# Optimization experiments

Hardware: AMD Instinct MI355X
Metric: run time of the kernel (lower is better)

The kernel has to match this reference:

```python
import jax, jax.numpy as jnp
import numpy as np

B, D, N = 8192, 1024, 4096     # batch, input_dim, num_outputs
SEG, W_SEG = 256, 16           # 256 uniform segments of width 16 (SEG*W_SEG == N)
TAU = 0.2                      # gumbel-softmax temperature


def setup_inputs() -> dict:
    key = jax.random.key(0)
    k1, k2, k3, k4 = jax.random.split(key, 4)
    bound = 1.0 / np.sqrt(D)   # init_bounded from the original module
    x = jax.random.normal(k1, (B, D), jnp.float32)
    W = jax.random.uniform(k2, (D, N), jnp.float32, -bound, bound)
    b = jax.random.uniform(k3, (N,), jnp.float32, -bound, bound)
    # Standard Gumbel(0,1) noise, precomputed for determinism: g = -log(-log(U))
    u = jax.random.uniform(k4, (B, N), jnp.float32, 1e-10, 1.0)
    gumbel = -jnp.log(-jnp.log(u))
    # segment flags: 0 -> tanh, nonzero -> gumbel-softmax (alternating)
    flags = (jnp.arange(SEG) % 2).astype(jnp.int32)
    return {"x": x, "W": W, "b": b, "gumbel": gumbel, "flags": flags}


def reference(x, W, b, gumbel, flags):
    # Dense layer
    outputs = x @ W + b                        # [B, N]
    # Segments are uniform-width, so the per-segment slice loop collapses to a reshape.
    y = outputs.reshape(B, SEG, W_SEG)         # [B, SEG, W_SEG]
    g = gumbel.reshape(B, SEG, W_SEG)
    # gumbel-softmax over each segment (hard=False path of the original)
    soft = jax.nn.softmax((y + g) / TAU, axis=-1)
    # per-segment dispatch: flag==0 -> tanh, else gumbel-softmax
    data_t = jnp.where(flags[None, :, None] == 0, jnp.tanh(y), soft)
    return outputs, data_t.reshape(B, N)
```

## Files before the change

kernel.cpp:

```cpp
#include <hip/hip_runtime.h>
#include <hip/hip_bf16.h>

#define B_DIM 8192
#define D_DIM 1024
#define N_DIM 4096
#define TAU_INV 5.0f

typedef __bf16 bf16x8 __attribute__((ext_vector_type(8)));
typedef __bf16 bf16x4 __attribute__((ext_vector_type(4)));
typedef float  f32x4  __attribute__((ext_vector_type(4)));

__device__ __forceinline__ void gld_lds16(const void* g, void* l) {
  __builtin_amdgcn_global_load_lds((const __attribute__((address_space(1))) void*)g,
                                   (__attribute__((address_space(3))) void*)l,
                                   16, 0, 0);
}
__device__ __forceinline__ float fast_rcp(float x) {
  return __builtin_amdgcn_rcpf(x);
}
#define MFMA(a, b, c) __builtin_amdgcn_mfma_f32_16x16x32_bf16((a), (b), (c), 0, 0, 0)

__global__ void prep_w(const float* __restrict__ W, __bf16* __restrict__ wht) {
  __shared__ float tile[32][33];
  const int tn = blockIdx.x & 127;
  const int tk = blockIdx.x >> 7;
  const int tx = threadIdx.x & 31;
  const int ty = threadIdx.x >> 5;
#pragma unroll
  for (int r = 0; r < 4; ++r) {
    const int k = tk * 32 + ty + r * 8;
    tile[ty + r * 8][tx] = W[(size_t)k * N_DIM + tn * 32 + tx];
  }
  __syncthreads();
#pragma unroll
  for (int r = 0; r < 4; ++r) {
    const int nn = tn * 32 + ty + r * 8;
    const int kk = tk * 32 + tx;
    wht[(size_t)nn * D_DIM + kk] = (__bf16)tile[tx][ty + r * 8];
  }
}

#define BM 128
#define BN 256
#define BK 32
#define THREADS 512

__global__ __launch_bounds__(THREADS, 4) void gemm_fused(
    const float* __restrict__ x,
    const __bf16* __restrict__ wht,
    const float* __restrict__ bias, const float* __restrict__ gumbel,
    const int* __restrict__ flags, float* __restrict__ out) {
  __shared__ __align__(16) __bf16 As[2][BM * BK];
  __shared__ __align__(16) __bf16 Bs[2][BN * BK];
  float* Ebuf = reinterpret_cast<float*>(&Bs[0][0]);

  const int tid  = threadIdx.x;
  const int lane = tid & 63;
  const int wave = tid >> 6;
  const int wr   = wave >> 2;
  const int wc   = wave & 3;
  const int fr   = lane & 15;
  const int q4   = lane >> 4;
  const int prot8 = ((q4 + ((fr >> 1) & 3)) & 3) * 8;

  const int bx  = blockIdx.x;
  const int xcd = bx & 7;
  const int ii  = bx >> 3;
  const int tn  = ii >> 3;
  const int tm  = xcd * 8 + (ii & 7);
  const int row0 = tm * BM;
  const int col0 = tn * BN;

  const int r0 = tid >> 2;
  const int l8 = (((tid & 3) - ((tid >> 3) & 3)) & 3) * 8;

  const float*  Axf = x   + (size_t)row0 * D_DIM;
  const __bf16* Bsc = wht + (size_t)col0 * D_DIM;

  f32x4 a0_, a1_;

#define ALOAD(t_)                                                            \
  do {                                                                       \
    const size_t o_ = (size_t)r0 * D_DIM + (t_) * 32 + l8;                   \
    a0_ = *reinterpret_cast<const f32x4*>(Axf + o_);                         \
    a1_ = *reinterpret_cast<const f32x4*>(Axf + o_ + 4);                     \
  } while (0)

#define CVTW(b)                                                              \
  do {                                                                       \
    bf16x8 h_;                                                               \
    h_[0] = (__bf16)a0_[0]; h_[1] = (__bf16)a0_[1];                          \
    h_[2] = (__bf16)a0_[2]; h_[3] = (__bf16)a0_[3];                          \
    h_[4] = (__bf16)a1_[0]; h_[5] = (__bf16)a1_[1];                          \
    h_[6] = (__bf16)a1_[2]; h_[7] = (__bf16)a1_[3];                          \
    *reinterpret_cast<bf16x8*>(&As[b][tid * 8]) = h_;                        \
  } while (0)

#define BGLD(b, t_)                                                          \
  do {                                                                       \
    const int ko_ = (t_) * 32;                                               \
    gld_lds16(Bsc + (size_t)r0 * D_DIM + ko_ + l8, &Bs[b][tid * 8]);         \
    gld_lds16(Bsc + (size_t)(128 + r0) * D_DIM + ko_ + l8,                   \
              &Bs[b][(512 + tid) * 8]);                                      \
  } while (0)

#define COMPUTE(b)                                                           \
  {                                                                          \
    bf16x8 bfr_[4];                                                          \
    _Pragma("unroll")                                                        \
    for (int n = 0; n < 4; ++n)                                              \
      bfr_[n] = *reinterpret_cast<const bf16x8*>(                            \
          &Bs[b][(wc * 64 + n * 16 + fr) * BK + prot8]);                     \
    __builtin_amdgcn_s_setprio(1);                                           \
    _Pragma("unroll")                                                        \
    for (int m = 0; m < 4; ++m) {                                            \
      const bf16x8 av_ = *reinterpret_cast<const bf16x8*>(                   \
          &As[b][(wr * 64 + m * 16 + fr) * BK + prot8]);                     \
      _Pragma("unroll")                                                      \
      for (int n = 0; n < 4; ++n)                                            \
        acc[m][n] = MFMA(bfr_[n], av_, acc[m][n]);                           \
    }                                                                        \
    __builtin_amdgcn_s_setprio(0);                                           \
  }

  f32x4 acc[4][4];
#pragma unroll
  for (int m = 0; m < 4; ++m)
#pragma unroll
    for (int n = 0; n < 4; ++n) acc[m][n] = (f32x4){0.f, 0.f, 0.f, 0.f};

  ALOAD(0);
  BGLD(0, 0);
  CVTW(0);
  __syncthreads();

#pragma unroll 1
  for (int it = 0; it < 15; ++it) {
    ALOAD(2 * it + 1); BGLD(1, 2 * it + 1);
    COMPUTE(0)
    CVTW(1);
    __syncthreads();
    ALOAD(2 * it + 2); BGLD(0, 2 * it + 2);
    COMPUTE(1)
    CVTW(0);
    __syncthreads();
  }
  ALOAD(31); BGLD(1, 31);
  COMPUTE(0)
  CVTW(1);
  __syncthreads();
  COMPUTE(1)

  float* out0 = out;
  float* out1 = out + (size_t)B_DIM * N_DIM;

  const int tcol = tid & 63;
  const int gcol = col0 + tcol * 4;
  const float4 bias4 = *reinterpret_cast<const float4*>(bias + gcol);
  const int flag = flags[(col0 >> 4) + (tcol >> 2)];

#pragma unroll
  for (int ck = 0; ck < 4; ++ck) {
    __syncthreads();
    if (wr == (ck >> 1)) {
#pragma unroll
      for (int mi = 0; mi < 2; ++mi) {
        const int lrow = mi * 16 + fr;
        const int m = (ck & 1) * 2 + mi;
#pragma unroll
        for (int n = 0; n < 4; ++n) {
          const int s = (wc * 16 + n * 4 + q4) ^ (lrow & 7);
          *reinterpret_cast<f32x4*>(&Ebuf[lrow * 256 + s * 4]) = acc[m][n];
        }
      }
    }
    __syncthreads();
#pragma unroll
    for (int rr = 0; rr < 4; ++rr) {
      const int lrow = rr * 8 + wave;
      const int grow = row0 + ck * 32 + lrow;
      const f32x4 a = *reinterpret_cast<const f32x4*>(
          &Ebuf[lrow * 256 + (tcol ^ (lrow & 7)) * 4]);
      const size_t idx = (size_t)grow * N_DIM + gcol;
      const float o0 = a[0] + bias4.x;
      const float o1 = a[1] + bias4.y;
      const float o2 = a[2] + bias4.z;
      const float o3 = a[3] + bias4.w;
      f32x4 ov = {o0, o1, o2, o3};
      __builtin_nontemporal_store(ov, reinterpret_cast<f32x4*>(out0 + idx));

      f32x4 v;
      if (flag == 0) {
        const float c0 = fminf(fmaxf(o0, -15.f), 15.f);
        const float c1 = fminf(fmaxf(o1, -15.f), 15.f);
        const float c2 = fminf(fmaxf(o2, -15.f), 15.f);
        const float c3 = fminf(fmaxf(o3, -15.f), 15.f);
        const float e0 = __expf(2.f * c0), e1 = __expf(2.f * c1);
        const float e2 = __expf(2.f * c2), e3 = __expf(2.f * c3);
        v[0] = (e0 - 1.f) * fast_rcp(e0 + 1.f);
        v[1] = (e1 - 1.f) * fast_rcp(e1 + 1.f);
        v[2] = (e2 - 1.f) * fast_rcp(e2 + 1.f);
        v[3] = (e3 - 1.f) * fast_rcp(e3 + 1.f);
      } else {
        const f32x4 g = __builtin_nontemporal_load(
            reinterpret_cast<const f32x4*>(gumbel + idx));
        const float t0 = (o0 + g[0]) * TAU_INV;
        const float t1 = (o1 + g[1]) * TAU_INV;
        const float t2 = (o2 + g[2]) * TAU_INV;
        const float t3 = (o3 + g[3]) * TAU_INV;
        float mx = fmaxf(fmaxf(t0, t1), fmaxf(t2, t3));
        mx = fmaxf(mx, __shfl_xor(mx, 1));
        mx = fmaxf(mx, __shfl_xor(mx, 2));
        const float e0 = __expf(t0 - mx), e1 = __expf(t1 - mx);
        const float e2 = __expf(t2 - mx), e3 = __expf(t3 - mx);
        float s = (e0 + e1) + (e2 + e3);
        s += __shfl_xor(s, 1);
        s += __shfl_xor(s, 2);
        const float inv = fast_rcp(s);
        v[0] = e0 * inv; v[1] = e1 * inv; v[2] = e2 * inv; v[3] = e3 * inv;
      }
      __builtin_nontemporal_store(v, reinterpret_cast<f32x4*>(out1 + idx));
    }
  }
}

__global__ void fallback_kernel(const float* __restrict__ x, const float* __restrict__ W,
                                const float* __restrict__ bias, const float* __restrict__ gumbel,
                                const int* __restrict__ flags, float* __restrict__ out) {
  const size_t idx = (size_t)blockIdx.x * blockDim.x + threadIdx.x;
  const int row = (int)(idx / N_DIM);
  const int col = (int)(idx % N_DIM);
  float o = bias[col];
  const float* xr = x + (size_t)row * D_DIM;
  for (int k = 0; k < D_DIM; ++k) o += xr[k] * W[(size_t)k * N_DIM + col];
  out[idx] = o;
  float v;
  if (flags[col >> 4] == 0) {
    const float oc = fminf(fmaxf(o, -15.f), 15.f);
    const float e2 = __expf(2.f * oc);
    v = (e2 - 1.f) / (e2 + 1.f);
  } else {
    const float t = (o + gumbel[idx]) * TAU_INV;
    float mx = t;
    mx = fmaxf(mx, __shfl_xor(mx, 1));
    mx = fmaxf(mx, __shfl_xor(mx, 2));
    mx = fmaxf(mx, __shfl_xor(mx, 4));
    mx = fmaxf(mx, __shfl_xor(mx, 8));
    float e = __expf(t - mx);
    float ssum = e;
    ssum += __shfl_xor(ssum, 1);
    ssum += __shfl_xor(ssum, 2);
    ssum += __shfl_xor(ssum, 4);
    ssum += __shfl_xor(ssum, 8);
    v = e / ssum;
  }
  out[(size_t)B_DIM * N_DIM + idx] = v;
}

extern "C" void kernel_launch(void* const* d_in, const int* in_sizes, int n_in,
                              void* d_out, int out_size, void* d_ws, size_t ws_size,
                              hipStream_t stream) {
  const float* x      = (const float*)d_in[0];
  const float* W      = (const float*)d_in[1];
  const float* bias   = (const float*)d_in[2];
  const float* gumbel = (const float*)d_in[3];
  const int*   flags  = (const int*)d_in[4];
  float* out = (float*)d_out;

  const size_t wcnt = (size_t)N_DIM * D_DIM;
  const size_t need = wcnt * sizeof(__bf16);

  if (ws_size < need) {
    const long long nblocks = (long long)B_DIM * N_DIM / 256;
    fallback_kernel<<<(int)nblocks, 256, 0, stream>>>(x, W, bias, gumbel, flags, out);
    return;
  }

  __bf16* wht = (__bf16*)d_ws;

  prep_w<<<(N_DIM / 32) * (D_DIM / 32), 256, 0, stream>>>(W, wht);
  gemm_fused<<<(B_DIM / BM) * (N_DIM / BN), THREADS, 0, stream>>>(
      x, wht, bias, gumbel, flags, out);
}
```

Before: 154.8 us.

## Make GEMM persistent over four column tiles and overlap epilogue with next mainloop

Result: slower. 228.7 us (+47.8%).

```diff
diff --git a/kernel.cpp b/kernel.cpp
--- a/kernel.cpp
+++ b/kernel.cpp
@@ -7,7 +7,6 @@
 #define TAU_INV 5.0f
 
 typedef __bf16 bf16x8 __attribute__((ext_vector_type(8)));
-typedef __bf16 bf16x4 __attribute__((ext_vector_type(4)));
 typedef float  f32x4  __attribute__((ext_vector_type(4)));
 
 __device__ __forceinline__ void gld_lds16(const void* g, void* l) {
@@ -45,14 +44,13 @@
 #define BK 32
 #define THREADS 512
 
-__global__ __launch_bounds__(THREADS, 4) void gemm_fused(
+__global__ __launch_bounds__(THREADS, 2) void gemm_fused(
     const float* __restrict__ x,
     const __bf16* __restrict__ wht,
     const float* __restrict__ bias, const float* __restrict__ gumbel,
     const int* __restrict__ flags, float* __restrict__ out) {
   __shared__ __align__(16) __bf16 As[2][BM * BK];
   __shared__ __align__(16) __bf16 Bs[2][BN * BK];
-  float* Ebuf = reinterpret_cast<float*>(&Bs[0][0]);
 
   const int tid  = threadIdx.x;
   const int lane = tid & 63;
@@ -66,18 +64,31 @@
   const int bx  = blockIdx.x;
   const int xcd = bx & 7;
   const int ii  = bx >> 3;
-  const int tn  = ii >> 3;
   const int tm  = xcd * 8 + (ii & 7);
+  const int tq  = ii >> 3;
   const int row0 = tm * BM;
-  const int col0 = tn * BN;
 
   const int r0 = tid >> 2;
   const int l8 = (((tid & 3) - ((tid >> 3) & 3)) & 3) * 8;
 
-  const float*  Axf = x   + (size_t)row0 * D_DIM;
-  const __bf16* Bsc = wht + (size_t)col0 * D_DIM;
+  const float* Axf = x + (size_t)row0 * D_DIM;
+  float* out0 = out;
+  float* out1 = out + (size_t)B_DIM * N_DIM;
+
+  f32x4 accA[4][4], accB[4][4];
+#pragma unroll
+  for (int m = 0; m < 4; ++m)
+#pragma unroll
+    for (int n = 0; n < 4; ++n) {
+      accA[m][n] = (f32x4){0.f, 0.f, 0.f, 0.f};
+      accB[m][n] = (f32x4){0.f, 0.f, 0.f, 0.f};
+    }
 
   f32x4 a0_, a1_;
+  f32x4 eg_, eb_;
+  size_t eix_ = 0;
+  int efl_ = 0;
+  int col0p = 0;
 
 #define ALOAD(t_)                                                            \
   do {                                                                       \
@@ -99,8 +110,8 @@
 #define BGLD(b, t_)                                                          \
   do {                                                                       \
     const int ko_ = (t_) * 32;                                               \
-    gld_lds16(Bsc + (size_t)r0 * D_DIM + ko_ + l8, &Bs[b][tid * 8]);         \
-    gld_lds16(Bsc + (size_t)(128 + r0) * D_DIM + ko_ + l8,                   \
+    gld_lds16(Bj + (size_t)r0 * D_DIM + ko_ + l8, &Bs[b][tid * 8]);          \
+    gld_lds16(Bj + (size_t)(128 + r0) * D_DIM + ko_ + l8,                    \
               &Bs[b][(512 + tid) * 8]);                                      \
   } while (0)
 
@@ -118,110 +129,132 @@
           &As[b][(wr * 64 + m * 16 + fr) * BK + prot8]);                     \
       _Pragma("unroll")                                                      \
       for (int n = 0; n < 4; ++n)                                            \
-        acc[m][n] = MFMA(bfr_[n], av_, acc[m][n]);                           \
+        accA[m][n] = MFMA(bfr_[n], av_, accA[m][n]);                         \
     }                                                                        \
     __builtin_amdgcn_s_setprio(0);                                           \
   }
 
-  f32x4 acc[4][4];
-#pragma unroll
-  for (int m = 0; m < 4; ++m)
-#pragma unroll
-    for (int n = 0; n < 4; ++n) acc[m][n] = (f32x4){0.f, 0.f, 0.f, 0.f};
-
-  ALOAD(0);
-  BGLD(0, 0);
-  CVTW(0);
+#define EPI_L(M, N)                                                          \
+  if (j) {                                                                   \
+    const int ec_ = col0p + wc * 64 + (N) * 16 + q4 * 4;                     \
+    const int er_ = row0 + wr * 64 + (M) * 16 + fr;                          \
+    eix_ = (size_t)er_ * N_DIM + ec_;                                        \
+    efl_ = flags[(col0p >> 4) + wc * 4 + (N)];                               \
+    eb_  = *reinterpret_cast<const f32x4*>(bias + ec_);                      \
+    if (efl_) eg_ = *reinterpret_cast<const f32x4*>(gumbel + eix_);          \
+  }
+
+#define EPI_U(M, N)                                                          \
+  if (j) {                                                                   \
+    const f32x4 o_ = accB[M][N] + eb_;                                       \
+    *reinterpret_cast<f32x4*>(out0 + eix_) = o_;                             \
+    f32x4 v_;                                                                \
+    if (!efl_) {                                                             \
+      _Pragma("unroll")                                                      \
+      for (int z = 0; z < 4; ++z) {                                          \
+        const float c_ = fminf(fmaxf(o_[z], -15.f), 15.f);                   \
+        const float e_ = __expf(2.f * c_);                                   \
+        v_[z] = (e_ - 1.f) * fast_rcp(e_ + 1.f);                             \
+      }                                                                      \
+    } else {                                                                 \
+      const float t0 = (o_[0] + eg_[0]) * TAU_INV;                           \
+      const float t1 = (o_[1] + eg_[1]) * TAU_INV;                           \
+      const float t2 = (o_[2] + eg_[2]) * TAU_INV;                           \
+      const float t3 = (o_[3] + eg_[3]) * TAU_INV;                           \
+      float mx = fmaxf(fmaxf(t0, t1), fmaxf(t2, t3));                        \
+      mx = fmaxf(mx, __shfl_xor(mx, 16));                                    \
+      mx = fmaxf(mx, __shfl_xor(mx, 32));                                    \
+      const float e0 = __expf(t0 - mx), e1 = __expf(t1 - mx);                \
+      const float e2 = __expf(t2 - mx), e3 = __expf(t3 - mx);                \
+      float s_ = (e0 + e1) + (e2 + e3);                                      \
+      s_ += __shfl_xor(s_, 16);                                              \
+      s_ += __shfl_xor(s_, 32);                                              \
+      const float iv_ = fast_rcp(s_);                                        \
+      v_[0] = e0 * iv_; v_[1] = e1 * iv_; v_[2] = e2 * iv_; v_[3] = e3 * iv_;\
+    }                                                                        \
+    *reinterpret_cast<f32x4*>(out1 + eix_) = v_;                             \
+  }
+
+#define STEPE(S, M, N)                                                       \
+  EPI_L(M, N)                                                                \
+  ALOAD((S) + 1); BGLD((((S) + 1) & 1), (S) + 1);                            \
+  COMPUTE(((S) & 1))                                                         \
+  EPI_U(M, N)                                                                \
+  CVTW((((S) + 1) & 1));                                                     \
   __syncthreads();
 
+#define STEPN(S)                                                             \
+  ALOAD((S) + 1); BGLD((((S) + 1) & 1), (S) + 1);                            \
+  COMPUTE(((S) & 1))                                                         \
+  CVTW((((S) + 1) & 1));                                                     \
+  __syncthreads();
+
 #pragma unroll 1
-  for (int it = 0; it < 15; ++it) {
-    ALOAD(2 * it + 1); BGLD(1, 2 * it + 1);
-    COMPUTE(0)
-    CVTW(1);
+  for (int j = 0; j < 4; ++j) {
+    const __bf16* Bj = wht + (size_t)(tq * 4 + j) * 256 * D_DIM;
+    const int col0j = (tq * 4 + j) * 256;
+    ALOAD(0); BGLD(0, 0); CVTW(0);
     __syncthreads();
-    ALOAD(2 * it + 2); BGLD(0, 2 * it + 2);
+    STEPE(0, 0, 0)  STEPE(1, 0, 1)  STEPE(2, 0, 2)  STEPE(3, 0, 3)
+    STEPE(4, 1, 0)  STEPE(5, 1, 1)  STEPE(6, 1, 2)  STEPE(7, 1, 3)
+    STEPE(8, 2, 0)  STEPE(9, 2, 1)  STEPE(10, 2, 2) STEPE(11, 2, 3)
+    STEPE(12, 3, 0) STEPE(13, 3, 1) STEPE(14, 3, 2) STEPE(15, 3, 3)
+    STEPN(16) STEPN(17) STEPN(18) STEPN(19) STEPN(20) STEPN(21) STEPN(22)
+    STEPN(23) STEPN(24) STEPN(25) STEPN(26) STEPN(27) STEPN(28) STEPN(29)
+    STEPN(30)
     COMPUTE(1)
-    CVTW(0);
-    __syncthreads();
-  }
-  ALOAD(31); BGLD(1, 31);
-  COMPUTE(0)
-  CVTW(1);
-  __syncthreads();
-  COMPUTE(1)
-
-  float* out0 = out;
-  float* out1 = out + (size_t)B_DIM * N_DIM;
-
-  const int tcol = tid & 63;
-  const int gcol = col0 + tcol * 4;
-  const float4 bias4 = *reinterpret_cast<const float4*>(bias + gcol);
-  const int flag = flags[(col0 >> 4) + (tcol >> 2)];
-
-#pragma unroll
-  for (int ck = 0; ck < 4; ++ck) {
-    __syncthreads();
-    if (wr == (ck >> 1)) {
-#pragma unroll
-      for (int mi = 0; mi < 2; ++mi) {
-        const int lrow = mi * 16 + fr;
-        const int m = (ck & 1) * 2 + mi;
-#pragma unroll
-        for (int n = 0; n < 4; ++n) {
-          const int s = (wc * 16 + n * 4 + q4) ^ (lrow & 7);
-          *reinterpret_cast<f32x4*>(&Ebuf[lrow * 256 + s * 4]) = acc[m][n];
-        }
+#pragma unroll
+    for (int m = 0; m < 4; ++m)
+#pragma unroll
+      for (int n = 0; n < 4; ++n) {
+        accB[m][n] = accA[m][n];
+        accA[m][n] = (f32x4){0.f, 0.f, 0.f, 0.f};
       }
-    }
-    __syncthreads();
-#pragma unroll
-    for (int rr = 0; rr < 4; ++rr) {
-      const int lrow = rr * 8 + wave;
-      const int grow = row0 + ck * 32 + lrow;
-      const f32x4 a = *reinterpret_cast<const f32x4*>(
-          &Ebuf[lrow * 256 + (tcol ^ (lrow & 7)) * 4]);
-      const size_t idx = (size_t)grow * N_DIM + gcol;
-      const float o0 = a[0] + bias4.x;
-      const float o1 = a[1] + bias4.y;
-      const float o2 = a[2] + bias4.z;
-      const float o3 = a[3] + bias4.w;
-      f32x4 ov = {o0, o1, o2, o3};
-      __builtin_nontemporal_store(ov, reinterpret_cast<f32x4*>(out0 + idx));
-
-      f32x4 v;
-      if (flag == 0) {
-        const float c0 = fminf(fmaxf(o0, -15.f), 15.f);
-        const float c1 = fminf(fmaxf(o1, -15.f), 15.f);
-        const float c2 = fminf(fmaxf(o2, -15.f), 15.f);
-        const float c3 = fminf(fmaxf(o3, -15.f), 15.f);
-        const float e0 = __expf(2.f * c0), e1 = __expf(2.f * c1);
-        const float e2 = __expf(2.f * c2), e3 = __expf(2.f * c3);
-        v[0] = (e0 - 1.f) * fast_rcp(e0 + 1.f);
-        v[1] = (e1 - 1.f) * fast_rcp(e1 + 1.f);
-        v[2] = (e2 - 1.f) * fast_rcp(e2 + 1.f);
-        v[3] = (e3 - 1.f) * fast_rcp(e3 + 1.f);
-      } else {
-        const f32x4 g = __builtin_nontemporal_load(
-            reinterpret_cast<const f32x4*>(gumbel + idx));
-        const float t0 = (o0 + g[0]) * TAU_INV;
-        const float t1 = (o1 + g[1]) * TAU_INV;
-        const float t2 = (o2 + g[2]) * TAU_INV;
-        const float t3 = (o3 + g[3]) * TAU_INV;
-        float mx = fmaxf(fmaxf(t0, t1), fmaxf(t2, t3));
-        mx = fmaxf(mx, __shfl_xor(mx, 1));
-        mx = fmaxf(mx, __shfl_xor(mx, 2));
-        const float e0 = __expf(t0 - mx), e1 = __expf(t1 - mx);
-        const float e2 = __expf(t2 - mx), e3 = __expf(t3 - mx);
-        float s = (e0 + e1) + (e2 + e3);
-        s += __shfl_xor(s, 1);
-        s += __shfl_xor(s, 2);
-        const float inv = fast_rcp(s);
-        v[0] = e0 * inv; v[1] = e1 * inv; v[2] = e2 * inv; v[3] = e3 * inv;
-      }
-      __builtin_nontemporal_store(v, reinterpret_cast<f32x4*>(out1 + idx));
-    }
-  }
+    col0p = col0j;
+  }
+
+#define DFRAG(M, N)                                                          \
+  {                                                                          \
+    const int ec_ = col0p + wc * 64 + (N) * 16 + q4 * 4;                     \
+    const int er_ = row0 + wr * 64 + (M) * 16 + fr;                          \
+    const size_t ix_ = (size_t)er_ * N_DIM + ec_;                            \
+    const int fl_ = flags[(col0p >> 4) + wc * 4 + (N)];                      \
+    const f32x4 bb_ = *reinterpret_cast<const f32x4*>(bias + ec_);           \
+    const f32x4 o_ = accB[M][N] + bb_;                                       \
+    __builtin_nontemporal_store(o_, reinterpret_cast<f32x4*>(out0 + ix_));   \
+    f32x4 v_;                                                                \
+    if (!fl_) {                                                              \
+      _Pragma("unroll")                                                      \
+      for (int z = 0; z < 4; ++z) {                                          \
+        const float c_ = fminf(fmaxf(o_[z], -15.f), 15.f);                   \
+        const float e_ = __expf(2.f * c_);                                   \
+        v_[z] = (e_ - 1.f) * fast_rcp(e_ + 1.f);                             \
+      }                                                                      \
+    } else {                                                                 \
+      const f32x4 g_ = __builtin_nontemporal_load(                           \
+          reinterpret_cast<const f32x4*>(gumbel + ix_));                     \
+      const float t0 = (o_[0] + g_[0]) * TAU_INV;                            \
+      const float t1 = (o_[1] + g_[1]) * TAU_INV;                            \
+      const float t2 = (o_[2] + g_[2]) * TAU_INV;                            \
+      const float t3 = (o_[3] + g_[3]) * TAU_INV;                            \
+      float mx = fmaxf(fmaxf(t0, t1), fmaxf(t2, t3));                        \
+      mx = fmaxf(mx, __shfl_xor(mx, 16));                                    \
+      mx = fmaxf(mx, __shfl_xor(mx, 32));                                    \
+      const float e0 = __expf(t0 - mx), e1 = __expf(t1 - mx);                \
+      const float e2 = __expf(t2 - mx), e3 = __expf(t3 - mx);                \
+      float s_ = (e0 + e1) + (e2 + e3);                                      \
+      s_ += __shfl_xor(s_, 16);                                              \
+      s_ += __shfl_xor(s_, 32);                                              \
+      const float iv_ = fast_rcp(s_);                                        \
+      v_[0] = e0 * iv_; v_[1] = e1 * iv_; v_[2] = e2 * iv_; v_[3] = e3 * iv_;\
+    }                                                                        \
+    __builtin_nontemporal_store(v_, reinterpret_cast<f32x4*>(out1 + ix_));   \
+  }
+
+  DFRAG(0, 0) DFRAG(0, 1) DFRAG(0, 2) DFRAG(0, 3)
+  DFRAG(1, 0) DFRAG(1, 1) DFRAG(1, 2) DFRAG(1, 3)
+  DFRAG(2, 0) DFRAG(2, 1) DFRAG(2, 2) DFRAG(2, 3)
+  DFRAG(3, 0) DFRAG(3, 1) DFRAG(3, 2) DFRAG(3, 3)
 }
 
 __global__ void fallback_kernel(const float* __restrict__ x, const float* __restrict__ W,
@@ -279,6 +312,5 @@
   __bf16* wht = (__bf16*)d_ws;
 
   prep_w<<<(N_DIM / 32) * (D_DIM / 32), 256, 0, stream>>>(W, wht);
-  gemm_fused<<<(B_DIM / BM) * (N_DIM / BN), THREADS, 0, stream>>>(
-      x, wht, bias, gumbel, flags, out);
-}
+  gemm_fused<<<256, THREADS, 0, stream>>>(x, wht, bias, gumbel, flags, out);
+}
```

## Split fused GEMM epilogue into separate GEMM-store and activation kernels

Applied to the files above, without the earlier changes.

Result: slower. 207.0 us (+33.7%).

```diff
diff --git a/kernel.cpp b/kernel.cpp
--- a/kernel.cpp
+++ b/kernel.cpp
@@ -7,7 +7,6 @@
 #define TAU_INV 5.0f
 
 typedef __bf16 bf16x8 __attribute__((ext_vector_type(8)));
-typedef __bf16 bf16x4 __attribute__((ext_vector_type(4)));
 typedef float  f32x4  __attribute__((ext_vector_type(4)));
 
 __device__ __forceinline__ void gld_lds16(const void* g, void* l) {
@@ -45,11 +44,10 @@
 #define BK 32
 #define THREADS 512
 
-__global__ __launch_bounds__(THREADS, 4) void gemm_fused(
+__global__ __launch_bounds__(THREADS, 4) void gemm_store(
     const float* __restrict__ x,
     const __bf16* __restrict__ wht,
-    const float* __restrict__ bias, const float* __restrict__ gumbel,
-    const int* __restrict__ flags, float* __restrict__ out) {
+    const float* __restrict__ bias, float* __restrict__ out0) {
   __shared__ __align__(16) __bf16 As[2][BM * BK];
   __shared__ __align__(16) __bf16 Bs[2][BN * BK];
   float* Ebuf = reinterpret_cast<float*>(&Bs[0][0]);
@@ -151,13 +149,9 @@
   __syncthreads();
   COMPUTE(1)
 
-  float* out0 = out;
-  float* out1 = out + (size_t)B_DIM * N_DIM;
-
   const int tcol = tid & 63;
   const int gcol = col0 + tcol * 4;
-  const float4 bias4 = *reinterpret_cast<const float4*>(bias + gcol);
-  const int flag = flags[(col0 >> 4) + (tcol >> 2)];
+  const f32x4 bias4 = *reinterpret_cast<const f32x4*>(bias + gcol);
 
 #pragma unroll
   for (int ck = 0; ck < 4; ++ck) {
@@ -181,47 +175,64 @@
       const int grow = row0 + ck * 32 + lrow;
       const f32x4 a = *reinterpret_cast<const f32x4*>(
           &Ebuf[lrow * 256 + (tcol ^ (lrow & 7)) * 4]);
-      const size_t idx = (size_t)grow * N_DIM + gcol;
-      const float o0 = a[0] + bias4.x;
-      const float o1 = a[1] + bias4.y;
-      const float o2 = a[2] + bias4.z;
-      const float o3 = a[3] + bias4.w;
-      f32x4 ov = {o0, o1, o2, o3};
-      __builtin_nontemporal_store(ov, reinterpret_cast<f32x4*>(out0 + idx));
-
-      f32x4 v;
-      if (flag == 0) {
-        const float c0 = fminf(fmaxf(o0, -15.f), 15.f);
-        const float c1 = fminf(fmaxf(o1, -15.f), 15.f);
-        const float c2 = fminf(fmaxf(o2, -15.f), 15.f);
-        const float c3 = fminf(fmaxf(o3, -15.f), 15.f);
-        const float e0 = __expf(2.f * c0), e1 = __expf(2.f * c1);
-        const float e2 = __expf(2.f * c2), e3 = __expf(2.f * c3);
-        v[0] = (e0 - 1.f) * fast_rcp(e0 + 1.f);
-        v[1] = (e1 - 1.f) * fast_rcp(e1 + 1.f);
-        v[2] = (e2 - 1.f) * fast_rcp(e2 + 1.f);
-        v[3] = (e3 - 1.f) * fast_rcp(e3 + 1.f);
-      } else {
-        const f32x4 g = __builtin_nontemporal_load(
-            reinterpret_cast<const f32x4*>(gumbel + idx));
-        const float t0 = (o0 + g[0]) * TAU_INV;
-        const float t1 = (o1 + g[1]) * TAU_INV;
-        const float t2 = (o2 + g[2]) * TAU_INV;
-        const float t3 = (o3 + g[3]) * TAU_INV;
-        float mx = fmaxf(fmaxf(t0, t1), fmaxf(t2, t3));
-        mx = fmaxf(mx, __shfl_xor(mx, 1));
-        mx = fmaxf(mx, __shfl_xor(mx, 2));
-        const float e0 = __expf(t0 - mx), e1 = __expf(t1 - mx);
-        const float e2 = __expf(t2 - mx), e3 = __expf(t3 - mx);
-        float s = (e0 + e1) + (e2 + e3);
-        s += __shfl_xor(s, 1);
-        s += __shfl_xor(s, 2);
-        const float inv = fast_rcp(s);
-        v[0] = e0 * inv; v[1] = e1 * inv; v[2] = e2 * inv; v[3] = e3 * inv;
-      }
-      __builtin_nontemporal_store(v, reinterpret_cast<f32x4*>(out1 + idx));
+      *reinterpret_cast<f32x4*>(out0 + (size_t)grow * N_DIM + gcol) = a + bias4;
     }
   }
+}
+
+__global__ __launch_bounds__(256) void act_kernel(
+    const float* __restrict__ o0, const float* __restrict__ gumbel,
+    const int* __restrict__ flags, float* __restrict__ out1) {
+  const int sid = blockIdx.x * 256 + threadIdx.x;
+  const int flag = flags[sid & 255];
+  const size_t base = (size_t)sid * 16;
+
+  f32x4 o[4];
+#pragma unroll
+  for (int i = 0; i < 4; ++i)
+    o[i] = *reinterpret_cast<const f32x4*>(o0 + base + i * 4);
+
+  f32x4 v[4];
+  if (flag == 0) {
+#pragma unroll
+    for (int i = 0; i < 4; ++i)
+#pragma unroll
+      for (int z = 0; z < 4; ++z) {
+        const float c = fminf(fmaxf(o[i][z], -15.f), 15.f);
+        const float e = __expf(2.f * c);
+        v[i][z] = (e - 1.f) * fast_rcp(e + 1.f);
+      }
+  } else {
+    f32x4 t[4];
+    float mx = -3.4e38f;
+#pragma unroll
+    for (int i = 0; i < 4; ++i) {
+      const f32x4 g = __builtin_nontemporal_load(
+          reinterpret_cast<const f32x4*>(gumbel + base + i * 4));
+#pragma unroll
+      for (int z = 0; z < 4; ++z) {
+        t[i][z] = (o[i][z] + g[z]) * TAU_INV;
+        mx = fmaxf(mx, t[i][z]);
+      }
+    }
+    float s = 0.f;
+#pragma unroll
+    for (int i = 0; i < 4; ++i)
+#pragma unroll
+      for (int z = 0; z < 4; ++z) {
+        t[i][z] = __expf(t[i][z] - mx);
+        s += t[i][z];
+      }
+    const float inv = fast_rcp(s);
+#pragma unroll
+    for (int i = 0; i < 4; ++i)
+#pragma unroll
+      for (int z = 0; z < 4; ++z) v[i][z] = t[i][z] * inv;
+  }
+#pragma unroll
+  for (int i = 0; i < 4; ++i)
+    __builtin_nontemporal_store(v[i],
+        reinterpret_cast<f32x4*>(out1 + base + i * 4));
 }
 
 __global__ void fallback_kernel(const float* __restrict__ x, const float* __restrict__ W,
@@ -277,8 +288,12 @@
   }
 
   __bf16* wht = (__bf16*)d_ws;
+  float* out0 = out;
+  float* out1 = out + (size_t)B_DIM * N_DIM;
 
   prep_w<<<(N_DIM / 32) * (D_DIM / 32), 256, 0, stream>>>(W, wht);
-  gemm_fused<<<(B_DIM / BM) * (N_DIM / BN), THREADS, 0, stream>>>(
-      x, wht, bias, gumbel, flags, out);
-}
+  gemm_store<<<(B_DIM / BM) * (N_DIM / BN), THREADS, 0, stream>>>(
+      x, wht, bias, out0);
+  act_kernel<<<(B_DIM * (N_DIM / 16)) / 256, 256, 0, stream>>>(
+      out0, gumbel, flags, out1);
+}
```
